# Performance work log

Hardware: AMD Instinct MI355X
Metric: run time of the kernel (lower is better)

Reference implementation:

```python
import jax, jax.numpy as jnp
import numpy as np

W = 0.5  # loss weight from __init__
EPS = 1e-14


def gradient_l2_loss(x):
    """Mean squared forward finite-difference along each spatial axis of (B,s,r,c)."""
    loss = 0.0
    for ax in (1, 2, 3):
        d = jnp.diff(x, axis=ax)
        loss = loss + jnp.mean(d * d)
    return loss


def setup_inputs() -> dict:
    key = jax.random.key(0)
    k1, k2 = jax.random.split(key)
    B, S, R, C = 2, 128, 128, 128
    L = jax.random.normal(k1, (B, 3, S, R, C), dtype=jnp.float32)
    U = jax.random.normal(k2, (B, 9, S, R, C), dtype=jnp.float32)
    return {"L": L, "U": U}


def reference(L, U):
    B, _, S, R, C = U.shape
    # torch.sort(L, dim=1, descending=True) -> indices[:,0] == argmax over the 3 eigenvalues
    idx0 = jnp.argmax(L, axis=1)  # (B,S,R,C) int
    # U channel layout U{row}_{col}: reshape to (B, col=3, row=3, S,R,C)
    Uview = U.reshape(B, 3, 3, S, R, C)
    idx = jnp.broadcast_to(idx0[:, None, None], (B, 3, 1, S, R, C))
    # faithful to original gather(dim=2)[:, :, 0]
    major = jnp.take_along_axis(Uview, idx, axis=2)[:, :, 0]  # (B,3,S,R,C)
    am = jnp.abs(major)
    den = jnp.sum(am * am, axis=1)  # (B,S,R,C)
    den = jnp.where(den < EPS, EPS, den)
    e1, e2, e3 = am[:, 0], am[:, 1], am[:, 2]
    CO = jnp.sqrt(0.5 * ((e1 - e2) ** 2 + (e2 - e3) ** 2 + (e3 - e1) ** 2) / den)
    CO_grad = 0.0
    for i in range(9):  # fixed small channel loop
        CO_grad = CO_grad + gradient_l2_loss(U[:, i])
    return (CO + CO_grad).mean() * W
```

## Files before the change

### kernel.cpp

```cpp
#include <hip/hip_runtime.h>

#define SS 128
#define RR 128
#define CC 128
#define RC (RR * CC)
#define LS 8
#define EPSF 1e-14f

__global__ __launch_bounds__(256, 2) void scol_main(const float* __restrict__ L,
                                                    const float* __restrict__ U,
                                                    float4* __restrict__ part,
                                                    int sChunks, int rChunks) {
    const int SRC = SS * RC;

    int tid  = threadIdx.x;
    int c4   = tid & 31;
    int rblk = tid >> 5;

    int g   = blockIdx.x;
    int sc  = g % sChunks;
    int rc  = (g / sChunks) % rChunks;
    int b   = g / (sChunks * rChunks);

    int r  = rc * 8 + rblk;
    int s0 = sc * LS;
    int c  = c4 << 2;

    bool  hr = (r < RR - 1), hc = (c4 < 31);
    float wr = hr ? 1.f : 0.f;
    float wc = hc ? 1.f : 0.f;
    int offr = hr ? CC : 0;

    int pos    = (s0 * RR + r) * CC + c;
    int base_l = b * 3 * SRC;
    int base_u = b * 9 * SRC;

    float4 ucur[9];
#pragma unroll
    for (int ch = 0; ch < 9; ++ch)
        ucur[ch] = *(const float4*)(U + base_u + ch * SRC + pos);

    float a_co = 0.f, a_ds = 0.f, a_dr = 0.f, a_dc = 0.f;

#pragma unroll 2
    for (int i = 0; i < LS; ++i) {
        int s = s0 + i;
        bool  hs  = (s < SS - 1);
        float wsf = hs ? 1.f : 0.f;
        int offn  = hs ? RC : 0;

        float4 l0 = *(const float4*)(L + base_l + pos);
        float4 l1 = *(const float4*)(L + base_l + SRC + pos);
        float4 l2 = *(const float4*)(L + base_l + 2 * SRC + pos);

        float4 urv[9], unx[9];
#pragma unroll
        for (int ch = 0; ch < 9; ++ch) {
            const float* p = U + base_u + ch * SRC + pos;
            urv[ch] = *(const float4*)(p + offr);
            unx[ch] = *(const float4*)(p + offn);
        }

        float L0[4] = {l0.x, l0.y, l0.z, l0.w};
        float L1[4] = {l1.x, l1.y, l1.z, l1.w};
        float L2[4] = {l2.x, l2.y, l2.z, l2.w};
        int idx[4];
#pragma unroll
        for (int j = 0; j < 4; ++j) {
            int id = 0;
            float best = L0[j];
            if (L1[j] > best) { best = L1[j]; id = 1; }
            if (L2[j] > best) { best = L2[j]; id = 2; }
            idx[j] = id;
        }

        float am[3][4];
#pragma unroll
        for (int gi = 0; gi < 3; ++gi)
#pragma unroll
            for (int j = 0; j < 4; ++j) am[gi][j] = 0.f;

        float t_dcb = 0.f, t_dr = 0.f, t_ds = 0.f;

#pragma unroll
        for (int ch = 0; ch < 9; ++ch) {
            float4 uu = ucur[ch];
            float uuv[4] = {uu.x, uu.y, uu.z, uu.w};
            int gi = ch / 3, m = ch % 3;
#pragma unroll
            for (int j = 0; j < 4; ++j)
                if (idx[j] == m) am[gi][j] = fabsf(uuv[j]);

            float d;
            d = uu.y - uu.x; a_dc += d * d;
            d = uu.z - uu.y; a_dc += d * d;
            d = uu.w - uu.z; a_dc += d * d;
            float un1 = __shfl_down(uu.x, 1);
            d = un1 - uu.w; t_dcb += d * d;

            float4 R4 = urv[ch];
            d = R4.x - uu.x; t_dr += d * d;
            d = R4.y - uu.y; t_dr += d * d;
            d = R4.z - uu.z; t_dr += d * d;
            d = R4.w - uu.w; t_dr += d * d;

            float4 S4 = unx[ch];
            d = S4.x - uu.x; t_ds += d * d;
            d = S4.y - uu.y; t_ds += d * d;
            d = S4.z - uu.z; t_ds += d * d;
            d = S4.w - uu.w; t_ds += d * d;

            ucur[ch] = S4;
        }
        a_dc += wc * t_dcb;
        a_dr += wr * t_dr;
        a_ds += wsf * t_ds;

#pragma unroll
        for (int j = 0; j < 4; ++j) {
            float e1 = am[0][j], e2 = am[1][j], e3 = am[2][j];
            float den = e1 * e1 + e2 * e2 + e3 * e3;
            den = fmaxf(den, EPSF);
            float num = 0.5f * ((e1 - e2) * (e1 - e2) + (e2 - e3) * (e2 - e3) +
                                (e3 - e1) * (e3 - e1));
            a_co += sqrtf(num / den);
        }

        pos += RC;
    }

#pragma unroll
    for (int off = 32; off > 0; off >>= 1) {
        a_co += __shfl_down(a_co, off);
        a_ds += __shfl_down(a_ds, off);
        a_dr += __shfl_down(a_dr, off);
        a_dc += __shfl_down(a_dc, off);
    }

    __shared__ float s_co[4], s_ds[4], s_dr[4], s_dc[4];
    int wid  = threadIdx.x >> 6;
    int lane = threadIdx.x & 63;
    if (lane == 0) {
        s_co[wid] = a_co; s_ds[wid] = a_ds;
        s_dr[wid] = a_dr; s_dc[wid] = a_dc;
    }
    __syncthreads();
    if (threadIdx.x == 0) {
        float t_co = 0.f, t_s = 0.f, t_r = 0.f, t_c = 0.f;
        for (int w = 0; w < 4; ++w) {
            t_co += s_co[w]; t_s += s_ds[w];
            t_r += s_dr[w]; t_c += s_dc[w];
        }
        part[blockIdx.x] = make_float4(t_co, t_s, t_r, t_c);
    }
}

__global__ __launch_bounds__(256) void scol_final(const float4* __restrict__ part,
                                                  float* __restrict__ out,
                                                  int nblk, int B) {
    double d_co = 0., d_ds = 0., d_dr = 0., d_dc = 0.;
    for (int i = threadIdx.x; i < nblk; i += blockDim.x) {
        float4 p = part[i];
        d_co += (double)p.x; d_ds += (double)p.y;
        d_dr += (double)p.z; d_dc += (double)p.w;
    }
#pragma unroll
    for (int off = 32; off > 0; off >>= 1) {
        d_co += __shfl_down(d_co, off);
        d_ds += __shfl_down(d_ds, off);
        d_dr += __shfl_down(d_dr, off);
        d_dc += __shfl_down(d_dc, off);
    }
    __shared__ double sh[4][4];
    int wid  = threadIdx.x >> 6;
    int lane = threadIdx.x & 63;
    if (lane == 0) {
        sh[wid][0] = d_co; sh[wid][1] = d_ds;
        sh[wid][2] = d_dr; sh[wid][3] = d_dc;
    }
    __syncthreads();
    if (threadIdx.x == 0) {
        double t_co = 0., t_ds = 0., t_dr = 0., t_dc = 0.;
        for (int w = 0; w < 4; ++w) {
            t_co += sh[w][0]; t_ds += sh[w][1];
            t_dr += sh[w][2]; t_dc += sh[w][3];
        }
        double nvox = (double)B * SS * RR * CC;
        double nds  = (double)B * (SS - 1) * RR * CC;
        double ndr  = (double)B * SS * (RR - 1) * CC;
        double ndc  = (double)B * SS * RR * (CC - 1);
        out[0] = (float)(0.5 * (t_co / nvox + t_ds / nds + t_dr / ndr + t_dc / ndc));
    }
}

extern "C" void kernel_launch(void* const* d_in, const int* in_sizes, int n_in,
                              void* d_out, int out_size, void* d_ws, size_t ws_size,
                              hipStream_t stream) {
    const float* L = (const float*)d_in[0];
    const float* U = (const float*)d_in[1];
    float* out = (float*)d_out;

    int B = in_sizes[1] / (9 * SS * RR * CC);
    int sChunks = SS / LS;
    int rChunks = RR / 8;
    int blocks  = B * sChunks * rChunks;

    float4* part = (float4*)d_ws;

    hipLaunchKernelGGL(scol_main, dim3(blocks), dim3(256), 0, stream,
                       L, U, part, sChunks, rChunks);
    hipLaunchKernelGGL(scol_final, dim3(1), dim3(256), 0, stream,
                       part, out, blocks, B);
}
```

Measured before the change: 256.1 us.

## Share row-neighbor values via cross-half-wave shuffles and shrink slice chunk

The even row of each wave now gets its r+1 neighbour from the odd row in the same wavefront through __shfl_down by 32. Only odd rows load the r+1 neighbour from global memory, which cuts redundant row-neighbour loads. The slice chunk per block is halved, the s-loop is fully unrolled and launch bounds request higher occupancy. The shuffle traffic and the divergent load branch add cost, and the smaller chunk causes more re-reads of the halo slice.

```diff
diff --git a/kernel.cpp b/kernel.cpp
--- a/kernel.cpp
+++ b/kernel.cpp
@@ -4,10 +4,10 @@
 #define RR 128
 #define CC 128
 #define RC (RR * CC)
-#define LS 8
+#define LS 4
 #define EPSF 1e-14f
 
-__global__ __launch_bounds__(256, 2) void scol_main(const float* __restrict__ L,
+__global__ __launch_bounds__(256, 4) void scol_main(const float* __restrict__ L,
                                                     const float* __restrict__ U,
                                                     float4* __restrict__ part,
                                                     int sChunks, int rChunks) {
@@ -16,20 +16,23 @@
     int tid  = threadIdx.x;
     int c4   = tid & 31;
     int rblk = tid >> 5;
-
-    int g   = blockIdx.x;
-    int sc  = g % sChunks;
-    int rc  = (g / sChunks) % rChunks;
-    int b   = g / (sChunks * rChunks);
+    bool odd = (rblk & 1);
+
+    int g  = blockIdx.x;
+    int sc = g % sChunks;
+    int rc = (g / sChunks) % rChunks;
+    int b  = g / (sChunks * rChunks);
 
     int r  = rc * 8 + rblk;
     int s0 = sc * LS;
     int c  = c4 << 2;
 
-    bool  hr = (r < RR - 1), hc = (c4 < 31);
-    float wr = hr ? 1.f : 0.f;
+    bool  hc = (c4 < 31);
     float wc = hc ? 1.f : 0.f;
-    int offr = hr ? CC : 0;
+    bool  hr = (r < RR - 1);
+    float wr_odd = hr ? 1.f : 0.f;
+    int   offr   = hr ? CC : 0;
+    float wrv    = odd ? wr_odd : 1.f;
 
     int pos    = (s0 * RR + r) * CC + c;
     int base_l = b * 3 * SRC;
@@ -42,7 +45,7 @@
 
     float a_co = 0.f, a_ds = 0.f, a_dr = 0.f, a_dc = 0.f;
 
-#pragma unroll 2
+#pragma unroll
     for (int i = 0; i < LS; ++i) {
         int s = s0 + i;
         bool  hs  = (s < SS - 1);
@@ -53,12 +56,16 @@
         float4 l1 = *(const float4*)(L + base_l + SRC + pos);
         float4 l2 = *(const float4*)(L + base_l + 2 * SRC + pos);
 
-        float4 urv[9], unx[9];
-#pragma unroll
-        for (int ch = 0; ch < 9; ++ch) {
-            const float* p = U + base_u + ch * SRC + pos;
-            urv[ch] = *(const float4*)(p + offr);
-            unx[ch] = *(const float4*)(p + offn);
+        float4 unx[9];
+#pragma unroll
+        for (int ch = 0; ch < 9; ++ch)
+            unx[ch] = *(const float4*)(U + base_u + ch * SRC + pos + offn);
+
+        float4 urg[9];
+        if (odd) {
+#pragma unroll
+            for (int ch = 0; ch < 9; ++ch)
+                urg[ch] = *(const float4*)(U + base_u + ch * SRC + pos + offr);
         }
 
         float L0[4] = {l0.x, l0.y, l0.z, l0.w};
@@ -98,7 +105,12 @@
             float un1 = __shfl_down(uu.x, 1);
             d = un1 - uu.w; t_dcb += d * d;
 
-            float4 R4 = urv[ch];
+            float4 Rsh;
+            Rsh.x = __shfl_down(uu.x, 32);
+            Rsh.y = __shfl_down(uu.y, 32);
+            Rsh.z = __shfl_down(uu.z, 32);
+            Rsh.w = __shfl_down(uu.w, 32);
+            float4 R4 = odd ? urg[ch] : Rsh;
             d = R4.x - uu.x; t_dr += d * d;
             d = R4.y - uu.y; t_dr += d * d;
             d = R4.z - uu.z; t_dr += d * d;
@@ -113,7 +125,7 @@
             ucur[ch] = S4;
         }
         a_dc += wc * t_dcb;
-        a_dr += wr * t_dr;
+        a_dr += wrv * t_dr;
         a_ds += wsf * t_ds;
 
 #pragma unroll
```

Result: slower. 644.4 us (+151.7%).
